# Performance work log

Measured on AMD Instinct MI355X. Metric: run time of the kernel, lower is better.

Reference implementation:

```python
import jax, jax.numpy as jnp
import numpy as np

BETA = 0.25


def setup_inputs() -> dict:
    key = jax.random.key(0)
    kx, ke = jax.random.split(key)
    x = jax.random.normal(kx, (32, 32, 32, 256), dtype=jnp.float32)
    embedding = jax.random.normal(ke, (256, 4096), dtype=jnp.float32) * 0.02
    return {"x": x, "embedding": embedding}


def reference(x, embedding):
    # x: [B, H, W, D]; embedding (codebook): [D, K]
    D = embedding.shape[0]
    flat = x.reshape(-1, D)                               # [N, D]
    sim = flat @ embedding                                # [N, K]
    dist = (jnp.sum(flat * flat, axis=1, keepdims=True)
            + jnp.sum(embedding * embedding, axis=0)
            - 2.0 * sim)                                  # [N, K]
    idx = jnp.argmin(dist, axis=1)                        # [N]
    # one-hot @ embedding.T  ==  gather rows of embedding.T
    quantized = jnp.take(embedding.T, idx, axis=0).reshape(x.shape)
    commitment_loss = BETA * jnp.mean((jax.lax.stop_gradient(quantized) - x) ** 2)
    codebook_loss = jnp.mean((quantized - jax.lax.stop_gradient(x)) ** 2)
    loss = commitment_loss + codebook_loss
    # straight-through estimator
    quantized_st = x + jax.lax.stop_gradient(quantized - x)
    return quantized_st, loss
```

## Files before the change

### kernel.cpp

```cpp
#include <hip/hip_runtime.h>
#include <math.h>

typedef _Float16 f16;
typedef f16 f16x8 __attribute__((ext_vector_type(8)));
typedef float f32x4 __attribute__((ext_vector_type(4)));

#define N_ROWS 32768
#define DIM    256
#define KCODES 4096

#define WS_ET    0
#define WS_BN    (WS_ET + KCODES*DIM)
#define WS_AN    (WS_BN + KCODES)
#define WS_PART  (WS_AN + N_ROWS)
#define WS_IDX   (WS_PART + 8192)
#define WS_BP    (WS_IDX + N_ROWS)
#define WS_AP    (WS_BP + 1048576)


__device__ __forceinline__ void gload16(const void* g, void* l) {
#if __has_builtin(__builtin_amdgcn_global_load_lds)
    __builtin_amdgcn_global_load_lds(
        (const __attribute__((address_space(1))) unsigned int*)g,
        (__attribute__((address_space(3))) unsigned int*)l, 16, 0, 0);
#else
    *(float4*)l = *(const float4*)g;
#endif
}

__global__ void vq_rownorm(const float* __restrict__ src, float* __restrict__ out, int nrows) {
    int w    = threadIdx.x >> 6;
    int lane = threadIdx.x & 63;
    int row  = blockIdx.x * 4 + w;
    if (row >= nrows) return;
    float4 v = *(const float4*)&src[row * DIM + lane * 4];
    float  s = v.x * v.x + v.y * v.y + v.z * v.z + v.w * v.w;
#pragma unroll
    for (int m = 1; m < 64; m <<= 1) s += __shfl_xor(s, m);
    if (lane == 0) out[row] = s;
}

__global__ void vq_prep_a(const float* __restrict__ x, char* __restrict__ Ap,
                          float* __restrict__ An) {
    const int t = threadIdx.x;
    const int lane = t & 63, w = t >> 6;
    const size_t row0 = (size_t)blockIdx.x * 128;
    char* base = Ap + (size_t)blockIdx.x * 131072;
    const int chunk = lane >> 4;
    const int dd2   = (lane & 15) * 8;
#pragma unroll 4
    for (int it = 0; it < 32; ++it) {
        const int m = it * 4 + w;
        float4 v = *(const float4*)&x[(row0 + m) * DIM + lane * 4];
        float vs[4] = { v.x, v.y, v.z, v.w };
        uint32_t hw[2], lw[2];
#pragma unroll
        for (int p = 0; p < 2; ++p) {
            uint32_t hword = 0, lword = 0;
#pragma unroll
            for (int j = 0; j < 2; ++j) {
                float s = vs[p * 2 + j] * 1024.0f;
                f16 h = (f16)s;
                f16 l = (f16)(s - (float)h);
                hword |= (uint32_t)__builtin_bit_cast(uint16_t, h) << (16 * j);
                lword |= (uint32_t)__builtin_bit_cast(uint16_t, l) << (16 * j);
            }
            hw[p] = hword; lw[p] = lword;
        }
        const int off = chunk * 16384 + m * 128 + (dd2 ^ ((m & 7) << 4));
        *(uint2*)(base + off)         = *(uint2*)hw;
        *(uint2*)(base + 65536 + off) = *(uint2*)lw;
        float s = v.x * v.x + v.y * v.y + v.z * v.z + v.w * v.w;
#pragma unroll
        for (int mm = 1; mm < 64; mm <<= 1) s += __shfl_xor(s, mm);
        if (lane == 0) An[row0 + m] = s;
    }
}

__global__ void vq_prep_b(const float* __restrict__ e, char* __restrict__ Bp,
                          float* __restrict__ et) {
    __shared__ float lt[128][65];
    const int t  = threadIdx.x;
    const int jb = blockIdx.x >> 2;
    const int c  = blockIdx.x & 3;
    const int d0 = c * 64, n0 = jb * 128;
#pragma unroll
    for (int it = 0; it < 8; ++it) {
        int linear = it * 256 + t;
        int drow = linear >> 5;
        int ncol = (linear & 31) * 4;
        float4 v = *(const float4*)&e[(size_t)(d0 + drow) * KCODES + n0 + ncol];
        lt[ncol + 0][drow] = v.x;
        lt[ncol + 1][drow] = v.y;
        lt[ncol + 2][drow] = v.z;
        lt[ncol + 3][drow] = v.w;
    }
    __syncthreads();
#pragma unroll
    for (int it = 0; it < 8; ++it) {
        int lin = it * 256 + t;
        int n = lin >> 4, q = lin & 15;
        float4 v = { lt[n][q*4], lt[n][q*4+1], lt[n][q*4+2], lt[n][q*4+3] };
        *(float4*)&et[(size_t)(n0 + n) * DIM + d0 + q * 4] = v;
    }
    char* ehbase = Bp + (size_t)jb * 131072 + c * 16384;
    const int n_loc = t >> 1;
    const int shalf = t & 1;
#pragma unroll
    for (int g = 0; g < 4; ++g) {
        const int dd8 = shalf * 32 + g * 8;
        uint32_t ehw[4], elw[4];
#pragma unroll
        for (int p = 0; p < 4; ++p) {
            uint32_t hword = 0, lword = 0;
#pragma unroll
            for (int j = 0; j < 2; ++j) {
                float s = lt[n_loc][dd8 + p * 2 + j] * 1024.0f;
                f16 h = (f16)s;
                f16 l = (f16)(s - (float)h);
                hword |= (uint32_t)__builtin_bit_cast(uint16_t, h) << (16 * j);
                lword |= (uint32_t)__builtin_bit_cast(uint16_t, l) << (16 * j);
            }
            ehw[p] = hword; elw[p] = lword;
        }
        const int off = n_loc * 128 + ((dd8 * 2) ^ ((n_loc & 7) << 4));
        *(uint4*)(ehbase + off)         = *(uint4*)ehw;
        *(uint4*)(ehbase + 65536 + off) = *(uint4*)elw;
    }
}

__global__ __launch_bounds__(512, 1) void vq_main(
    const char* __restrict__ Ap, const char* __restrict__ Bp,
    const float* __restrict__ An, const float* __restrict__ Bn,
    int* __restrict__ idxOut)
{
    __shared__ __align__(16) char LaH[2][16384];
    __shared__ __align__(16) char LaL[16384];
    __shared__ __align__(16) char LbEH[32768];
    __shared__ __align__(16) char LbEL[32768];
    __shared__ unsigned long long red[128][4];

    const int tid = threadIdx.x;
    const int wid = tid >> 6, lane = tid & 63;
    const int wr = wid >> 2, wc = wid & 3;
    const int hi = lane >> 4, ln = lane & 15;
    const int sx = (lane & 7) << 4;
    const size_t row0 = (size_t)blockIdx.x * 128;
    const char* abase = Ap + (size_t)blockIdx.x * 131072;

    float an[16];
#pragma unroll
    for (int mi = 0; mi < 4; ++mi)
#pragma unroll
        for (int r = 0; r < 4; ++r)
            an[mi * 4 + r] = An[row0 + wr * 64 + mi * 16 + hi * 4 + r];

    unsigned long long run[16];
#pragma unroll
    for (int v = 0; v < 16; ++v) run[v] = ~0ull;

#define ISSUE_X(t)                                                            \
    do {                                                                      \
        const int c_ = (t) & 3;                                               \
        gload16(abase + 65536 + c_ * 16384 + tid * 16,        LaL + tid * 16);\
        gload16(abase + 65536 + c_ * 16384 + 8192 + tid * 16,                 \
                LaL + 8192 + tid * 16);                                       \
        const int tn_ = ((t) + 1) & 63;                                       \
        const int cn_ = tn_ & 3;                                              \
        char* ah_ = (char*)LaH[tn_ & 1];                                      \
        gload16(abase + cn_ * 16384 + tid * 16,        ah_ + tid * 16);       \
        gload16(abase + cn_ * 16384 + 8192 + tid * 16, ah_ + 8192 + tid * 16);\
    } while (0)

#define ISSUE_Y(t)                                                            \
    do {                                                                      \
        const int tn = ((t) + 1) & 63;                                        \
        const int c_ = tn & 3, it_ = tn >> 2;                                 \
        const char* b0_ = Bp + (size_t)(2 * it_) * 131072;                    \
        const char* b1_ = b0_ + 131072;                                       \
        gload16(b0_ + c_ * 16384 + tid * 16,        LbEH + tid * 16);         \
        gload16(b0_ + c_ * 16384 + 8192 + tid * 16, LbEH + 8192 + tid * 16);  \
        gload16(b1_ + c_ * 16384 + tid * 16,        LbEH + 16384 + tid * 16); \
        gload16(b1_ + c_ * 16384 + 8192 + tid * 16, LbEH + 24576 + tid * 16); \
        gload16(b0_ + 65536 + c_ * 16384 + tid * 16,        LbEL + tid * 16); \
        gload16(b0_ + 65536 + c_ * 16384 + 8192 + tid * 16,                   \
                LbEL + 8192 + tid * 16);                                      \
        gload16(b1_ + 65536 + c_ * 16384 + tid * 16,                          \
                LbEL + 16384 + tid * 16);                                     \
        gload16(b1_ + 65536 + c_ * 16384 + 8192 + tid * 16,                   \
                LbEL + 24576 + tid * 16);                                     \
    } while (0)

    f32x4 acc[4][4] = {};

    {
        char* ah_ = (char*)LaH[0];
        gload16(abase + tid * 16,        ah_ + tid * 16);
        gload16(abase + 8192 + tid * 16, ah_ + 8192 + tid * 16);
        const char* b0_ = Bp;
        const char* b1_ = Bp + 131072;
        gload16(b0_ + tid * 16,        LbEH + tid * 16);
        gload16(b0_ + 8192 + tid * 16, LbEH + 8192 + tid * 16);
        gload16(b1_ + tid * 16,        LbEH + 16384 + tid * 16);
        gload16(b1_ + 8192 + tid * 16, LbEH + 24576 + tid * 16);
        gload16(b0_ + 65536 + tid * 16,        LbEL + tid * 16);
        gload16(b0_ + 65536 + 8192 + tid * 16, LbEL + 8192 + tid * 16);
        gload16(b1_ + 65536 + tid * 16,        LbEL + 16384 + tid * 16);
        gload16(b1_ + 65536 + 8192 + tid * 16, LbEL + 24576 + tid * 16);
    }

#pragma unroll 1
    for (int t = 0; t < 64; ++t) {
        ISSUE_X(t);
        asm volatile("s_waitcnt vmcnt(4)" ::: "memory");
        __builtin_amdgcn_s_barrier();
        __builtin_amdgcn_sched_barrier(0);

        const char* ah = LaH[t & 1];
        f16x8 aH[8], bH[8], bL[8];
#pragma unroll
        for (int ks = 0; ks < 2; ++ks) {
            const int ko = (ks * 64 + hi * 16) ^ sx;
#pragma unroll
            for (int i = 0; i < 4; ++i)
                aH[ks * 4 + i] = *(const f16x8*)(ah + (wr * 64 + i * 16 + ln) * 128 + ko);
#pragma unroll
            for (int ni = 0; ni < 4; ++ni) {
                const int brow = ((wc & 1) * 64 + ni * 16 + ln) * 128 + ko;
                bH[ks * 4 + ni] = *(const f16x8*)(LbEH + (wc >> 1) * 16384 + brow);
                bL[ks * 4 + ni] = *(const f16x8*)(LbEL + (wc >> 1) * 16384 + brow);
            }
        }
        __builtin_amdgcn_s_setprio(1);
#pragma unroll
        for (int ks = 0; ks < 2; ++ks)
#pragma unroll
            for (int mi = 0; mi < 4; ++mi)
#pragma unroll
                for (int ni = 0; ni < 4; ++ni)
                    acc[mi][ni] = __builtin_amdgcn_mfma_f32_16x16x32_f16(
                        aH[ks * 4 + mi], bH[ks * 4 + ni], acc[mi][ni], 0, 0, 0);
#pragma unroll
        for (int ks = 0; ks < 2; ++ks)
#pragma unroll
            for (int mi = 0; mi < 4; ++mi)
#pragma unroll
                for (int ni = 0; ni < 4; ++ni)
                    acc[mi][ni] = __builtin_amdgcn_mfma_f32_16x16x32_f16(
                        aH[ks * 4 + mi], bL[ks * 4 + ni], acc[mi][ni], 0, 0, 0);
        __builtin_amdgcn_s_setprio(0);
        __builtin_amdgcn_s_barrier();

        ISSUE_Y(t);
        asm volatile("s_waitcnt vmcnt(10)" ::: "memory");
        __builtin_amdgcn_s_barrier();
        __builtin_amdgcn_sched_barrier(0);

        f16x8 aL[8];
#pragma unroll
        for (int ks = 0; ks < 2; ++ks) {
            const int ko = (ks * 64 + hi * 16) ^ sx;
#pragma unroll
            for (int i = 0; i < 4; ++i)
                aL[ks * 4 + i] = *(const f16x8*)(LaL + (wr * 64 + i * 16 + ln) * 128 + ko);
        }
        __builtin_amdgcn_s_setprio(1);
#pragma unroll
        for (int ks = 0; ks < 2; ++ks)
#pragma unroll
            for (int mi = 0; mi < 4; ++mi)
#pragma unroll
                for (int ni = 0; ni < 4; ++ni)
                    acc[mi][ni] = __builtin_amdgcn_mfma_f32_16x16x32_f16(
                        aL[ks * 4 + mi], bH[ks * 4 + ni], acc[mi][ni], 0, 0, 0);
        __builtin_amdgcn_s_setprio(0);
        __builtin_amdgcn_s_barrier();

        if ((t & 3) == 3) {
            const int it = t >> 2;
            float bn[4];
#pragma unroll
            for (int ni = 0; ni < 4; ++ni)
                bn[ni] = Bn[it * 256 + wc * 64 + ni * 16 + ln];
#pragma unroll
            for (int mi = 0; mi < 4; ++mi)
#pragma unroll
                for (int r = 0; r < 4; ++r) {
                    const float a = an[mi * 4 + r];
                    unsigned long long best = run[mi * 4 + r];
#pragma unroll
                    for (int ni = 0; ni < 4; ++ni) {
                        float sim  = acc[mi][ni][r] * 0x1p-20f;
                        float tt   = a + bn[ni];
                        float dist = tt - 2.0f * sim;
                        unsigned code = (unsigned)(it * 256 + wc * 64 + ni * 16 + ln);
                        unsigned long long p =
                            ((unsigned long long)__float_as_uint(dist) << 32) | code;
                        best = p < best ? p : best;
                    }
                    run[mi * 4 + r] = best;
                }
#pragma unroll
            for (int mi = 0; mi < 4; ++mi)
#pragma unroll
                for (int ni = 0; ni < 4; ++ni)
                    acc[mi][ni] = f32x4{0.f, 0.f, 0.f, 0.f};
        }
    }
#undef ISSUE_X
#undef ISSUE_Y

#pragma unroll
    for (int v = 0; v < 16; ++v) {
#pragma unroll
        for (int m = 1; m < 16; m <<= 1) {
            unsigned long long o = __shfl_xor(run[v], m);
            run[v] = o < run[v] ? o : run[v];
        }
    }
    if (ln == 0) {
#pragma unroll
        for (int mi = 0; mi < 4; ++mi)
#pragma unroll
            for (int r = 0; r < 4; ++r)
                red[wr * 64 + mi * 16 + hi * 4 + r][wc] = run[mi * 4 + r];
    }
    __syncthreads();
    if (tid < 128) {
        unsigned long long b = red[tid][0];
#pragma unroll
        for (int w = 1; w < 4; ++w) {
            unsigned long long o = red[tid][w];
            b = o < b ? o : b;
        }
        idxOut[row0 + tid] = (int)(unsigned)(b & 0xffffffffull);
    }
}

__global__ void vq_gather(const float* __restrict__ x, const float* __restrict__ et,
                          const int* __restrict__ idx,
                          float* __restrict__ out, float* __restrict__ part) {
    __shared__ float wsum[4];
    int w    = threadIdx.x >> 6;
    int lane = threadIdx.x & 63;
    int row  = blockIdx.x * 4 + w;
    int k    = idx[row];
    float4 q  = *(const float4*)&et[(size_t)k * DIM + lane * 4];
    float4 xv = *(const float4*)&x[(size_t)row * DIM + lane * 4];
    *(float4*)&out[(size_t)row * DIM + lane * 4] = q;
    float d0 = q.x - xv.x, d1 = q.y - xv.y, d2 = q.z - xv.z, d3 = q.w - xv.w;
    float s = d0 * d0 + d1 * d1 + d2 * d2 + d3 * d3;
#pragma unroll
    for (int m = 1; m < 64; m <<= 1) s += __shfl_xor(s, m);
    if (lane == 0) wsum[w] = s;
    __syncthreads();
    if (threadIdx.x == 0) part[blockIdx.x] = wsum[0] + wsum[1] + wsum[2] + wsum[3];
}

__global__ void vq_finalize(const float* __restrict__ part, float* __restrict__ lossOut) {
    __shared__ float sm[256];
    float s = 0.0f;
    for (int i = threadIdx.x; i < 8192; i += 256) s += part[i];
    sm[threadIdx.x] = s;
    __syncthreads();
    for (int st = 128; st > 0; st >>= 1) {
        if (threadIdx.x < st) sm[threadIdx.x] += sm[threadIdx.x + st];
        __syncthreads();
    }
    if (threadIdx.x == 0)
        lossOut[0] = 1.25f * (sm[0] / 8388608.0f);
}

extern "C" void kernel_launch(void* const* d_in, const int* in_sizes, int n_in,
                              void* d_out, int out_size, void* d_ws, size_t ws_size,
                              hipStream_t stream) {
    const float* x = (const float*)d_in[0];
    const float* e = (const float*)d_in[1];
    float* out = (float*)d_out;
    float* ws  = (float*)d_ws;

    float* et   = ws + WS_ET;
    float* bn   = ws + WS_BN;
    float* an   = ws + WS_AN;
    float* part = ws + WS_PART;
    int*   idx  = (int*)(ws + WS_IDX);
    char*  Bp   = (char*)(ws + WS_BP);
    char*  Ap   = (char*)(ws + WS_AP);

    vq_prep_a<<<256, 256, 0, stream>>>(x, Ap, an);
    vq_prep_b<<<128, 256, 0, stream>>>(e, Bp, et);
    vq_rownorm<<<KCODES / 4, 256, 0, stream>>>(et, bn, KCODES);
    vq_main<<<256, 512, 0, stream>>>(Ap, Bp, an, bn, idx);
    vq_gather<<<N_ROWS / 4, 256, 0, stream>>>(x, et, idx, out, part);
    vq_finalize<<<1, 256, 0, stream>>>(part, out + (size_t)N_ROWS * DIM);
}
```

Baseline: 276.7 us.

## Restructure VQ GEMM main loop into six-phase pipeline with double-buffered LDS

The split-fp16 distance GEMM loop is reorganized into six phases per K-chunk. Each phase issues its MFMAs while the LDS fragments for the next phase are read, and global-to-LDS loads are spread across the phases. A-high, A-low and B-high tiles are now double-buffered, and the reduction scratch array reuses the B-low LDS region so the added buffers fit in shared memory. The aim is to hide LDS read latency and global load latency behind MFMA work, at the cost of more barriers and higher LDS and register pressure.

```diff
diff --git a/kernel.cpp b/kernel.cpp
--- a/kernel.cpp
+++ b/kernel.cpp
@@ -135,16 +135,17 @@
     int* __restrict__ idxOut)
 {
     __shared__ __align__(16) char LaH[2][16384];
-    __shared__ __align__(16) char LaL[16384];
-    __shared__ __align__(16) char LbEH[32768];
+    __shared__ __align__(16) char LaL[2][16384];
+    __shared__ __align__(16) char LbEH[2][32768];
     __shared__ __align__(16) char LbEL[32768];
-    __shared__ unsigned long long red[128][4];
 
     const int tid = threadIdx.x;
     const int wid = tid >> 6, lane = tid & 63;
     const int wr = wid >> 2, wc = wid & 3;
     const int hi = lane >> 4, ln = lane & 15;
     const int sx = (lane & 7) << 4;
+    const int ko0 = (hi * 16) ^ sx;
+    const int ko1 = (64 + hi * 16) ^ sx;
     const size_t row0 = (size_t)blockIdx.x * 128;
     const char* abase = Ap + (size_t)blockIdx.x * 131072;
 
@@ -159,29 +160,36 @@
 #pragma unroll
     for (int v = 0; v < 16; ++v) run[v] = ~0ull;
 
-#define ISSUE_X(t)                                                            \
+#define ISSUE_E1(tn)                                                          \
     do {                                                                      \
-        const int c_ = (t) & 3;                                               \
-        gload16(abase + 65536 + c_ * 16384 + tid * 16,        LaL + tid * 16);\
+        const int c_ = (tn) & 3, sl_ = (tn) & 1;                              \
+        gload16(abase + c_ * 16384 + tid * 16,        LaH[sl_] + tid * 16);   \
+        gload16(abase + c_ * 16384 + 8192 + tid * 16,                         \
+                LaH[sl_] + 8192 + tid * 16);                                  \
+        gload16(abase + 65536 + c_ * 16384 + tid * 16, LaL[sl_] + tid * 16);  \
         gload16(abase + 65536 + c_ * 16384 + 8192 + tid * 16,                 \
-                LaL + 8192 + tid * 16);                                       \
-        const int tn_ = ((t) + 1) & 63;                                       \
-        const int cn_ = tn_ & 3;                                              \
-        char* ah_ = (char*)LaH[tn_ & 1];                                      \
-        gload16(abase + cn_ * 16384 + tid * 16,        ah_ + tid * 16);       \
-        gload16(abase + cn_ * 16384 + 8192 + tid * 16, ah_ + 8192 + tid * 16);\
+                LaL[sl_] + 8192 + tid * 16);                                  \
     } while (0)
 
-#define ISSUE_Y(t)                                                            \
+#define ISSUE_E2(tn)                                                          \
     do {                                                                      \
-        const int tn = ((t) + 1) & 63;                                        \
-        const int c_ = tn & 3, it_ = tn >> 2;                                 \
+        const int c_ = (tn) & 3, it_ = (tn) >> 2, sl_ = (tn) & 1;             \
         const char* b0_ = Bp + (size_t)(2 * it_) * 131072;                    \
         const char* b1_ = b0_ + 131072;                                       \
-        gload16(b0_ + c_ * 16384 + tid * 16,        LbEH + tid * 16);         \
-        gload16(b0_ + c_ * 16384 + 8192 + tid * 16, LbEH + 8192 + tid * 16);  \
-        gload16(b1_ + c_ * 16384 + tid * 16,        LbEH + 16384 + tid * 16); \
-        gload16(b1_ + c_ * 16384 + 8192 + tid * 16, LbEH + 24576 + tid * 16); \
+        gload16(b0_ + c_ * 16384 + tid * 16,        LbEH[sl_] + tid * 16);    \
+        gload16(b0_ + c_ * 16384 + 8192 + tid * 16,                           \
+                LbEH[sl_] + 8192 + tid * 16);                                 \
+        gload16(b1_ + c_ * 16384 + tid * 16,                                  \
+                LbEH[sl_] + 16384 + tid * 16);                                \
+        gload16(b1_ + c_ * 16384 + 8192 + tid * 16,                           \
+                LbEH[sl_] + 24576 + tid * 16);                                \
+    } while (0)
+
+#define ISSUE_L(tn)                                                           \
+    do {                                                                      \
+        const int c_ = (tn) & 3, it_ = (tn) >> 2;                             \
+        const char* b0_ = Bp + (size_t)(2 * it_) * 131072;                    \
+        const char* b1_ = b0_ + 131072;                                       \
         gload16(b0_ + 65536 + c_ * 16384 + tid * 16,        LbEL + tid * 16); \
         gload16(b0_ + 65536 + c_ * 16384 + 8192 + tid * 16,                   \
                 LbEL + 8192 + tid * 16);                                      \
@@ -191,90 +199,87 @@
                 LbEL + 24576 + tid * 16);                                     \
     } while (0)
 
+#define READ_A(dst, buf, koo)                                                 \
+    _Pragma("unroll")                                                         \
+    for (int i_ = 0; i_ < 4; ++i_)                                            \
+        dst[i_] = *(const f16x8*)((buf) + (wr * 64 + i_ * 16 + ln) * 128 + (koo));
+
+#define READ_B(dst, buf, koo)                                                 \
+    _Pragma("unroll")                                                         \
+    for (int n_ = 0; n_ < 4; ++n_)                                            \
+        dst[n_] = *(const f16x8*)((buf) + ((wc & 1) * 64 + n_ * 16 + ln) * 128 + (koo));
+
+#define LGKM_FENCE()                                                          \
+    asm volatile("s_waitcnt lgkmcnt(0)" ::: "memory");                        \
+    __builtin_amdgcn_sched_barrier(0)
+
+#define MFMA16(A, B)                                                          \
+    __builtin_amdgcn_s_setprio(1);                                            \
+    _Pragma("unroll")                                                         \
+    for (int mi_ = 0; mi_ < 4; ++mi_)                                         \
+        _Pragma("unroll")                                                     \
+        for (int ni_ = 0; ni_ < 4; ++ni_)                                     \
+            acc[mi_][ni_] = __builtin_amdgcn_mfma_f32_16x16x32_f16(           \
+                A[mi_], B[ni_], acc[mi_][ni_], 0, 0, 0);                      \
+    __builtin_amdgcn_s_setprio(0)
+
     f32x4 acc[4][4] = {};
-
-    {
-        char* ah_ = (char*)LaH[0];
-        gload16(abase + tid * 16,        ah_ + tid * 16);
-        gload16(abase + 8192 + tid * 16, ah_ + 8192 + tid * 16);
-        const char* b0_ = Bp;
-        const char* b1_ = Bp + 131072;
-        gload16(b0_ + tid * 16,        LbEH + tid * 16);
-        gload16(b0_ + 8192 + tid * 16, LbEH + 8192 + tid * 16);
-        gload16(b1_ + tid * 16,        LbEH + 16384 + tid * 16);
-        gload16(b1_ + 8192 + tid * 16, LbEH + 24576 + tid * 16);
-        gload16(b0_ + 65536 + tid * 16,        LbEL + tid * 16);
-        gload16(b0_ + 65536 + 8192 + tid * 16, LbEL + 8192 + tid * 16);
-        gload16(b1_ + 65536 + tid * 16,        LbEL + 16384 + tid * 16);
-        gload16(b1_ + 65536 + 8192 + tid * 16, LbEL + 24576 + tid * 16);
-    }
+    f16x8 aH0[4], aH1[4], bH0[4], bH1[4], bl[4], al[4];
+
+    ISSUE_E1(0);
+    ISSUE_E2(0);
+    ISSUE_L(0);
+    asm volatile("s_waitcnt vmcnt(4)" ::: "memory");
+    __builtin_amdgcn_s_barrier();
+    READ_A(aH0, LaH[0], ko0);
+    READ_B(bH0, LbEH[0] + (wc >> 1) * 16384, ko0);
 
 #pragma unroll 1
     for (int t = 0; t < 64; ++t) {
-        ISSUE_X(t);
+        const int s  = t & 1;
+        const int tn = (t + 1) & 63;
+        const int sn = tn & 1;
+        const char* aHb = LaH[s];
+        const char* aLb = LaL[s];
+        const char* bHb = LbEH[s] + (wc >> 1) * 16384;
+        const char* bLb = LbEL + (wc >> 1) * 16384;
+
+        __builtin_amdgcn_s_barrier();
+        ISSUE_E1(tn);
+        LGKM_FENCE();
+        MFMA16(aH0, bH0);
+        READ_A(aH1, aHb, ko1);
+        READ_B(bH1, bHb, ko1);
+
         asm volatile("s_waitcnt vmcnt(4)" ::: "memory");
         __builtin_amdgcn_s_barrier();
-        __builtin_amdgcn_sched_barrier(0);
-
-        const char* ah = LaH[t & 1];
-        f16x8 aH[8], bH[8], bL[8];
-#pragma unroll
-        for (int ks = 0; ks < 2; ++ks) {
-            const int ko = (ks * 64 + hi * 16) ^ sx;
-#pragma unroll
-            for (int i = 0; i < 4; ++i)
-                aH[ks * 4 + i] = *(const f16x8*)(ah + (wr * 64 + i * 16 + ln) * 128 + ko);
-#pragma unroll
-            for (int ni = 0; ni < 4; ++ni) {
-                const int brow = ((wc & 1) * 64 + ni * 16 + ln) * 128 + ko;
-                bH[ks * 4 + ni] = *(const f16x8*)(LbEH + (wc >> 1) * 16384 + brow);
-                bL[ks * 4 + ni] = *(const f16x8*)(LbEL + (wc >> 1) * 16384 + brow);
-            }
-        }
-        __builtin_amdgcn_s_setprio(1);
-#pragma unroll
-        for (int ks = 0; ks < 2; ++ks)
-#pragma unroll
-            for (int mi = 0; mi < 4; ++mi)
-#pragma unroll
-                for (int ni = 0; ni < 4; ++ni)
-                    acc[mi][ni] = __builtin_amdgcn_mfma_f32_16x16x32_f16(
-                        aH[ks * 4 + mi], bH[ks * 4 + ni], acc[mi][ni], 0, 0, 0);
-#pragma unroll
-        for (int ks = 0; ks < 2; ++ks)
-#pragma unroll
-            for (int mi = 0; mi < 4; ++mi)
-#pragma unroll
-                for (int ni = 0; ni < 4; ++ni)
-                    acc[mi][ni] = __builtin_amdgcn_mfma_f32_16x16x32_f16(
-                        aH[ks * 4 + mi], bL[ks * 4 + ni], acc[mi][ni], 0, 0, 0);
-        __builtin_amdgcn_s_setprio(0);
-        __builtin_amdgcn_s_barrier();
-
-        ISSUE_Y(t);
-        asm volatile("s_waitcnt vmcnt(10)" ::: "memory");
-        __builtin_amdgcn_s_barrier();
-        __builtin_amdgcn_sched_barrier(0);
-
-        f16x8 aL[8];
-#pragma unroll
-        for (int ks = 0; ks < 2; ++ks) {
-            const int ko = (ks * 64 + hi * 16) ^ sx;
-#pragma unroll
-            for (int i = 0; i < 4; ++i)
-                aL[ks * 4 + i] = *(const f16x8*)(LaL + (wr * 64 + i * 16 + ln) * 128 + ko);
-        }
-        __builtin_amdgcn_s_setprio(1);
-#pragma unroll
-        for (int ks = 0; ks < 2; ++ks)
-#pragma unroll
-            for (int mi = 0; mi < 4; ++mi)
-#pragma unroll
-                for (int ni = 0; ni < 4; ++ni)
-                    acc[mi][ni] = __builtin_amdgcn_mfma_f32_16x16x32_f16(
-                        aL[ks * 4 + mi], bH[ks * 4 + ni], acc[mi][ni], 0, 0, 0);
-        __builtin_amdgcn_s_setprio(0);
-        __builtin_amdgcn_s_barrier();
+        ISSUE_E2(tn);
+        LGKM_FENCE();
+        MFMA16(aH1, bH1);
+        READ_B(bl, bLb, ko0);
+
+        __builtin_amdgcn_s_barrier();
+        LGKM_FENCE();
+        MFMA16(aH0, bl);
+        READ_B(bl, bLb, ko1);
+
+        __builtin_amdgcn_s_barrier();
+        LGKM_FENCE();
+        MFMA16(aH1, bl);
+        READ_A(al, aLb, ko0);
+
+        __builtin_amdgcn_s_barrier();
+        ISSUE_L(tn);
+        LGKM_FENCE();
+        MFMA16(al, bH0);
+        READ_A(al, aLb, ko1);
+
+        asm volatile("s_waitcnt vmcnt(4)" ::: "memory");
+        __builtin_amdgcn_s_barrier();
+        LGKM_FENCE();
+        MFMA16(al, bH1);
+        READ_A(aH0, LaH[sn], ko0);
+        READ_B(bH0, LbEH[sn] + (wc >> 1) * 16384, ko0);
 
         if ((t & 3) == 3) {
             const int it = t >> 2;
@@ -307,8 +312,13 @@
                     acc[mi][ni] = f32x4{0.f, 0.f, 0.f, 0.f};
         }
     }
-#undef ISSUE_X
-#undef ISSUE_Y
+#undef ISSUE_E1
+#undef ISSUE_E2
+#undef ISSUE_L
+#undef READ_A
+#undef READ_B
+#undef LGKM_FENCE
+#undef MFMA16
 
 #pragma unroll
     for (int v = 0; v < 16; ++v) {
@@ -318,6 +328,8 @@
             run[v] = o < run[v] ? o : run[v];
         }
     }
+    __syncthreads();
+    unsigned long long (*red)[4] = (unsigned long long (*)[4])LbEL;
     if (ln == 0) {
 #pragma unroll
         for (int mi = 0; mi < 4; ++mi)
```

New measurement: 242.5 us. 1.14x faster.
